# Kernel optimization log

Measured on AMD Instinct MI355X. Metric: run time of the kernel, lower is better.

The kernel has to match this reference:

```python
import jax, jax.numpy as jnp
import numpy as np

NUM_HEADS = 32
NUM_KV = 8
Q_MULT = NUM_HEADS // NUM_KV  # 4
HEAD_DIM = 128
WINDOW = 1024
SM_SCALE = 1.0 / np.sqrt(HEAD_DIM)


def setup_inputs() -> dict:
    key = jax.random.key(0)
    k1, k2, k3, k4 = jax.random.split(key, 4)
    B, S = 2, 2048
    Q = jax.random.normal(k1, (B, S, NUM_HEADS * HEAD_DIM), dtype=jnp.float32)
    K = jax.random.normal(k2, (B, S, NUM_KV * HEAD_DIM), dtype=jnp.float32)
    V = jax.random.normal(k3, (B, S, NUM_KV * HEAD_DIM), dtype=jnp.float32)
    sinks = jax.random.normal(k4, (NUM_HEADS,), dtype=jnp.float32) * 0.1
    return {"Q": Q, "K": K, "V": V, "sinks": sinks}


def reference(Q, K, V, sinks):
    B, S, _ = Q.shape
    # GQA layout: head = kv * q_mult + m (matches Q[b].view(S, kv, q_mult, d))
    Qh = Q.reshape(B, S, NUM_KV, Q_MULT, HEAD_DIM)
    Kh = K.reshape(B, S, NUM_KV, HEAD_DIM)
    Vh = V.reshape(B, S, NUM_KV, HEAD_DIM)

    # scores: [B, kv, q_mult, S_q, S_k]
    scores = jnp.einsum('bqhmd,bkhd->bhmqk', Qh, Kh) * SM_SCALE

    q_idx = jnp.arange(S)[:, None]
    k_idx = jnp.arange(S)[None, :]
    # causal AND within sliding window: q - WINDOW < k <= q
    allowed = (k_idx <= q_idx) & (k_idx > q_idx - WINDOW)
    scores = jnp.where(allowed[None, None, None, :, :], scores, -jnp.inf)

    # learned sink logit per head, appended as an extra softmax column
    sink = sinks.reshape(NUM_KV, Q_MULT)[None, :, :, None, None]
    sink = jnp.broadcast_to(sink, (B, NUM_KV, Q_MULT, S, 1))
    logits = jnp.concatenate([scores, sink], axis=-1)
    w = jax.nn.softmax(logits, axis=-1)[..., :-1]  # drop sink column

    out = jnp.einsum('bhmqk,bkhd->bqhmd', w, Vh)
    return out.reshape(B, S, NUM_HEADS * HEAD_DIM)
```

## Files before the change

### kernel.cpp

```cpp
#include <hip/hip_runtime.h>
#include <stdint.h>

#define S_LEN 2048
#define HD    128
#define NKV   8
#define NQM   4
#define WIN   1024
#define QB    32
#define KTILE 32
#define KVROW (NKV * HD)
#define QROW  (NQM * NKV * HD)

typedef __attribute__((ext_vector_type(8))) short bf16x8;
typedef __attribute__((ext_vector_type(4))) float f32x4;
typedef __attribute__((ext_vector_type(4))) int   i32x4;

__device__ __forceinline__ uint32_t cvtpk(float lo, float hi) {
  uint32_t r;
  asm("v_cvt_pk_bf16_f32 %0, %1, %2" : "=v"(r) : "v"(lo), "v"(hi));
  return r;
}
__device__ __forceinline__ uint32_t perm2(uint32_t a, uint32_t b, uint32_t sel) {
  uint32_t r;
  asm("v_perm_b32 %0, %1, %2, %3" : "=v"(r) : "v"(a), "v"(b), "s"(sel));
  return r;
}

__device__ __forceinline__ void load8bf(const uint16_t* p, uint32_t o[4]) {
  i32x4 v = *reinterpret_cast<const i32x4*>(p);
  o[0] = (uint32_t)v[0]; o[1] = (uint32_t)v[1]; o[2] = (uint32_t)v[2]; o[3] = (uint32_t)v[3];
}
__device__ __forceinline__ void load8bf(const float* p, uint32_t o[4]) {
  float4 a = *reinterpret_cast<const float4*>(p);
  float4 b = *reinterpret_cast<const float4*>(p + 4);
  o[0] = cvtpk(a.x, a.y);
  o[1] = cvtpk(a.z, a.w);
  o[2] = cvtpk(b.x, b.y);
  o[3] = cvtpk(b.z, b.w);
}

__global__ void cvt2_kernel(const float* __restrict__ inK, const float* __restrict__ inV,
                            uint16_t* __restrict__ outK, uint16_t* __restrict__ outV, int n4) {
  int i = blockIdx.x * blockDim.x + threadIdx.x;
  int stride = gridDim.x * blockDim.x;
  for (int j = i; j < 2 * n4; j += stride) {
    const float* in = (j < n4) ? inK : inV;
    uint16_t* out   = (j < n4) ? outK : outV;
    int jj = (j < n4) ? j : j - n4;
    float4 v = reinterpret_cast<const float4*>(in)[jj];
    uint2 o;
    o.x = cvtpk(v.x, v.y);
    o.y = cvtpk(v.z, v.w);
    reinterpret_cast<uint2*>(out)[jj] = o;
  }
}

#define VSWZ(d) (((((uint32_t)(d) >> 3) ^ (uint32_t)(d)) & 7u) << 3)

#define KPERM(a)  ((((a) >> 2) & 3) * 8 + ((a) >> 4) * 4 + ((a) & 3))
#define KPERMI(k) ((((k) >> 2) & 1) * 16 + ((k) >> 3) * 4 + ((k) & 3))

template <typename KVT>
__launch_bounds__(256, 2)
__global__ void attn_kernel(const float* __restrict__ Q,
                            const KVT* __restrict__ Ksrc,
                            const KVT* __restrict__ Vsrc,
                            const float* __restrict__ sinks,
                            float* __restrict__ out) {
  __shared__ __align__(16) uint8_t smem[32768];

  const int tid  = threadIdx.x;
  const int lane = tid & 63;
  const int wv   = tid >> 6;
  const int c    = lane & 15;
  const int g    = lane >> 4;

  const int bid = blockIdx.x;
  const int kv  = bid & 7;
  const int i2  = bid >> 3;
  const int b   = i2 / 48;
  const int pairIdx = i2 % 48;
  const int head = kv * NQM + wv;
  const float sink_l2 = sinks[head] * 1.4426950408889634f;

  int qtA, qtB, nrep;
  if (pairIdx < 16) { qtA = 31 - pairIdx; qtB = pairIdx; nrep = 2; }
  else              { qtA = pairIdx + 16; qtB = 0;       nrep = 1; }

  const size_t kbase = (size_t)(b * S_LEN) * KVROW + kv * HD;
  uint32_t kgo[2];
  #pragma unroll
  for (int ch = 0; ch < 2; ++ch) {
    const int o    = wv * 2048 + ch * 1024 + lane * 16;
    const int row  = o >> 8;
    const int key  = KPERM(row);
    const int scol = (o & 255) ^ ((row & 7) << 4);
    kgo[ch] = (uint32_t)(key * (KVROW * 2) + scol);
  }
  const int kr  = tid >> 3;
  const int kcB = (tid & 7) * 32;
  const int kpr = KPERMI(kr);
  const uint32_t kw0 = (uint32_t)(kpr * 256 + ((kcB)      ^ ((kpr & 7) << 4)));
  const uint32_t kw1 = (uint32_t)(kpr * 256 + ((kcB + 16) ^ ((kpr & 7) << 4)));
  const KVT* kg = Ksrc + kbase + (tid & 7) * 16;
  const int va = tid >> 4;
  const int vd = tid & 15;
  const KVT* vg = Vsrc + kbase + vd * 8;

  uint32_t vr0[4], vr1[4];

  auto stageK = [&](uint8_t* kbuf, int kt) {
    if constexpr (sizeof(KVT) == 2) {
      const uint8_t* kb = (const uint8_t*)(Ksrc + kbase) + (size_t)kt * (KVROW * 2);
      #pragma unroll
      for (int ch = 0; ch < 2; ++ch) {
        __builtin_amdgcn_global_load_lds(
            (const __attribute__((address_space(1))) void*)(kb + kgo[ch]),
            (__attribute__((address_space(3))) void*)(kbuf + wv * 2048 + ch * 1024),
            16, 0, 0);
      }
    } else {
      const KVT* src = kg + (size_t)(kt + kr) * KVROW;
      uint32_t t0[4], t1[4];
      load8bf(src, t0); load8bf(src + 8, t1);
      i32x4 w0, w1;
      w0[0]=(int)t0[0]; w0[1]=(int)t0[1]; w0[2]=(int)t0[2]; w0[3]=(int)t0[3];
      w1[0]=(int)t1[0]; w1[1]=(int)t1[1]; w1[2]=(int)t1[2]; w1[3]=(int)t1[3];
      *reinterpret_cast<i32x4*>(kbuf + kw0) = w0;
      *reinterpret_cast<i32x4*>(kbuf + kw1) = w1;
    }
  };
  auto loadV = [&](int kt) {
    const KVT* vs = vg + (size_t)(kt + 2 * va) * KVROW;
    load8bf(vs, vr0); load8bf(vs + KVROW, vr1);
  };
  auto writeV = [&](uint8_t* vbuf) {
    #pragma unroll
    for (int ii = 0; ii < 8; ++ii) {
      int d = vd * 8 + ii;
      uint32_t w = (ii & 1) ? perm2(vr1[ii >> 1], vr0[ii >> 1], 0x07060302u)
                            : perm2(vr1[ii >> 1], vr0[ii >> 1], 0x05040100u);
      uint32_t byte = (uint32_t)(d * 64) + (((uint32_t)(va * 4)) ^ VSWZ(d));
      *reinterpret_cast<uint32_t*>(vbuf + byte) = w;
    }
  };

  const float SCALE2 = 0.08838834764831845f * 1.4426950408889634f;

  for (int rep = 0; rep < nrep; ++rep) {
    const int q0 = (rep ? qtB : qtA) * QB;

    bf16x8 qf[2][4];
    #pragma unroll
    for (int tq = 0; tq < 2; ++tq) {
      const float* qp = Q + (size_t)(b * S_LEN + q0 + tq * 16 + c) * QROW + head * HD;
      #pragma unroll
      for (int f = 0; f < 4; ++f) {
        int d0 = f * 32 + g * 8;
        float4 a = *reinterpret_cast<const float4*>(qp + d0);
        float4 bb = *reinterpret_cast<const float4*>(qp + d0 + 4);
        i32x4 t;
        t[0] = (int)cvtpk(a.x * SCALE2, a.y * SCALE2);
        t[1] = (int)cvtpk(a.z * SCALE2, a.w * SCALE2);
        t[2] = (int)cvtpk(bb.x * SCALE2, bb.y * SCALE2);
        t[3] = (int)cvtpk(bb.z * SCALE2, bb.w * SCALE2);
        qf[tq][f] = __builtin_bit_cast(bf16x8, t);
      }
    }

    float m_[2] = {sink_l2, sink_l2};
    float lp_[2] = {0.25f, 0.25f};
    f32x4 acc[2][8];
    #pragma unroll
    for (int tq = 0; tq < 2; ++tq)
      #pragma unroll
      for (int dt = 0; dt < 8; ++dt) acc[tq][dt] = (f32x4)0.0f;

    int kstart = q0 - (WIN - 1);
    if (kstart < 0) kstart = 0;
    kstart &= ~(KTILE - 1);

    uint8_t* kcur = smem;         uint8_t* kalt = smem + 8192;
    uint8_t* vcur = smem + 16384; uint8_t* valt = smem + 24576;

    loadV(kstart);
    stageK(kcur, kstart);
    writeV(vcur);
    __syncthreads();

    for (int kt = kstart; kt <= q0; kt += KTILE) {
      const int ktn = (kt + KTILE <= q0) ? (kt + KTILE) : kt;
      stageK(kalt, ktn);
      loadV(ktn);

      f32x4 st[2][2];
      #pragma unroll
      for (int a_ = 0; a_ < 2; ++a_)
        #pragma unroll
        for (int b_ = 0; b_ < 2; ++b_) st[a_][b_] = (f32x4)0.0f;

      __builtin_amdgcn_s_setprio(1);
      #pragma unroll
      for (int kt_ = 0; kt_ < 2; ++kt_) {
        bf16x8 kf[4];
        #pragma unroll
        for (int f = 0; f < 4; ++f) {
          int row = kt_ * 16 + c;
          uint32_t byte = (uint32_t)(row * 256 + ((f * 64 + g * 16) ^ ((row & 7) << 4)));
          kf[f] = *reinterpret_cast<const bf16x8*>(kcur + byte);
        }
        #pragma unroll
        for (int tq = 0; tq < 2; ++tq)
          #pragma unroll
          for (int f = 0; f < 4; ++f)
            st[kt_][tq] = __builtin_amdgcn_mfma_f32_16x16x32_bf16(kf[f], qf[tq][f], st[kt_][tq], 0, 0, 0);
      }
      __builtin_amdgcn_s_setprio(0);

      const bool need_mask = (kt + KTILE - 1 > q0) || (kt < q0 + QB - WIN);
      if (need_mask) {
        #pragma unroll
        for (int kt_ = 0; kt_ < 2; ++kt_)
          #pragma unroll
          for (int tq = 0; tq < 2; ++tq)
            #pragma unroll
            for (int r = 0; r < 4; ++r) {
              int k_ = kt + g * 8 + kt_ * 4 + r;
              int q_ = q0 + tq * 16 + c;
              bool ok = (k_ <= q_) && (k_ > q_ - WIN);
              if (!ok) st[kt_][tq][r] = -1e38f;
            }
      }

      bf16x8 pa[2];
      #pragma unroll
      for (int tq = 0; tq < 2; ++tq) {
        float ownmax = fmaxf(fmaxf(fmaxf(st[0][tq][0], st[0][tq][1]), fmaxf(st[0][tq][2], st[0][tq][3])),
                             fmaxf(fmaxf(st[1][tq][0], st[1][tq][1]), fmaxf(st[1][tq][2], st[1][tq][3])));
        const float mold = m_[tq];
        if (!__all(ownmax <= mold + 11.54f)) {
          float vmax = fmaxf(ownmax, __shfl_xor(ownmax, 16));
          vmax = fmaxf(vmax, __shfl_xor(vmax, 32));
          float mnew = fmaxf(mold, vmax);
          float scl  = exp2f(mold - mnew);
          m_[tq] = mnew;
          lp_[tq] *= scl;
          float sc[4];
          #pragma unroll
          for (int r = 0; r < 4; ++r) sc[r] = __shfl(scl, (lane & 48) | (g * 4 + r));
          #pragma unroll
          for (int dt = 0; dt < 8; ++dt)
            #pragma unroll
            for (int r = 0; r < 4; ++r) acc[tq][dt][r] *= sc[r];
        }
        const float mrun = m_[tq];
        float p[2][4];
        float s = 0.0f;
        #pragma unroll
        for (int kt_ = 0; kt_ < 2; ++kt_)
          #pragma unroll
          for (int r = 0; r < 4; ++r) {
            float e = exp2f(st[kt_][tq][r] - mrun);
            p[kt_][r] = e;
            s += e;
          }
        lp_[tq] += s;
        i32x4 pv;
        pv[0] = (int)cvtpk(p[0][0], p[0][1]);
        pv[1] = (int)cvtpk(p[0][2], p[0][3]);
        pv[2] = (int)cvtpk(p[1][0], p[1][1]);
        pv[3] = (int)cvtpk(p[1][2], p[1][3]);
        pa[tq] = __builtin_bit_cast(bf16x8, pv);
      }

      __builtin_amdgcn_s_setprio(1);
      #pragma unroll
      for (int dt = 0; dt < 8; ++dt) {
        int d = dt * 16 + c;
        uint32_t rowb = (uint32_t)(d * 64);
        uint32_t swz  = VSWZ(d);
        uint2 lo = *reinterpret_cast<const uint2*>(vcur + rowb + (((uint32_t)(g * 16))     ^ swz));
        uint2 hi = *reinterpret_cast<const uint2*>(vcur + rowb + (((uint32_t)(g * 16 + 8)) ^ swz));
        i32x4 vv; vv[0] = (int)lo.x; vv[1] = (int)lo.y; vv[2] = (int)hi.x; vv[3] = (int)hi.y;
        bf16x8 vf = __builtin_bit_cast(bf16x8, vv);
        #pragma unroll
        for (int tq = 0; tq < 2; ++tq)
          acc[tq][dt] = __builtin_amdgcn_mfma_f32_16x16x32_bf16(pa[tq], vf, acc[tq][dt], 0, 0, 0);
      }
      __builtin_amdgcn_s_setprio(0);

      writeV(valt);
      __syncthreads();
      uint8_t* t0 = kcur; kcur = kalt; kalt = t0;
      uint8_t* t1 = vcur; vcur = valt; valt = t1;
    }

    #pragma unroll
    for (int tq = 0; tq < 2; ++tq) {
      float lt = lp_[tq];
      lt += __shfl_xor(lt, 16);
      lt += __shfl_xor(lt, 32);
      float linv = 1.0f / lt;
      float li[4];
      #pragma unroll
      for (int r = 0; r < 4; ++r) li[r] = __shfl(linv, (lane & 48) | (g * 4 + r));
      #pragma unroll
      for (int dt = 0; dt < 8; ++dt)
        #pragma unroll
        for (int r = 0; r < 4; ++r) {
          size_t o = (size_t)(b * S_LEN + q0 + tq * 16 + g * 4 + r) * QROW + head * HD + dt * 16 + c;
          out[o] = acc[tq][dt][r] * li[r];
        }
    }
  }
}

extern "C" void kernel_launch(void* const* d_in, const int* in_sizes, int n_in,
                              void* d_out, int out_size, void* d_ws, size_t ws_size,
                              hipStream_t stream) {
  const float* Q     = (const float*)d_in[0];
  const float* K     = (const float*)d_in[1];
  const float* V     = (const float*)d_in[2];
  const float* sinks = (const float*)d_in[3];
  float* out = (float*)d_out;

  const int nK = in_sizes[1];
  const int B  = in_sizes[0] / (S_LEN * QROW);
  dim3 grid(384 * B);

  const size_t need = (size_t)nK * 2u * 2u;
  if (ws_size >= need) {
    uint16_t* Kb = (uint16_t*)d_ws;
    uint16_t* Vb = Kb + nK;
    cvt2_kernel<<<1024, 256, 0, stream>>>(K, V, Kb, Vb, nK / 4);
    attn_kernel<uint16_t><<<grid, 256, 0, stream>>>(Q, Kb, Vb, sinks, out);
  } else {
    attn_kernel<float><<<grid, 256, 0, stream>>>(Q, K, V, sinks, out);
  }
}
```

Measured before the change: 219.1 us.

## Stage V via direct global-to-LDS loads and read with transposing LDS loads

V tiles are now copied straight from global memory into LDS with global_load_lds, in a new row layout, replacing the register round trip that used byte permutes and scattered 32-bit stores. The PV MFMA operands are then read with ds_read_b64_tr_b16 transposing LDS loads, software-pipelined one step ahead with explicit lgkmcnt waits. The aim is to cut VALU and LDS-write work and register pressure in the main loop. The hand-written waitcnt and sched barriers add scheduling rigidity, and the bf16 path relies on the new layout matching the transpose read pattern exactly.

```diff
diff --git a/kernel.cpp b/kernel.cpp
--- a/kernel.cpp
+++ b/kernel.cpp
@@ -14,15 +14,11 @@
 typedef __attribute__((ext_vector_type(8))) short bf16x8;
 typedef __attribute__((ext_vector_type(4))) float f32x4;
 typedef __attribute__((ext_vector_type(4))) int   i32x4;
+typedef __attribute__((ext_vector_type(2))) unsigned u32x2;
 
 __device__ __forceinline__ uint32_t cvtpk(float lo, float hi) {
   uint32_t r;
   asm("v_cvt_pk_bf16_f32 %0, %1, %2" : "=v"(r) : "v"(lo), "v"(hi));
-  return r;
-}
-__device__ __forceinline__ uint32_t perm2(uint32_t a, uint32_t b, uint32_t sel) {
-  uint32_t r;
-  asm("v_perm_b32 %0, %1, %2, %3" : "=v"(r) : "v"(a), "v"(b), "s"(sel));
   return r;
 }
 
@@ -55,10 +51,9 @@
   }
 }
 
-#define VSWZ(d) (((((uint32_t)(d) >> 3) ^ (uint32_t)(d)) & 7u) << 3)
-
 #define KPERM(a)  ((((a) >> 2) & 3) * 8 + ((a) >> 4) * 4 + ((a) & 3))
 #define KPERMI(k) ((((k) >> 2) & 1) * 16 + ((k) >> 3) * 4 + ((k) & 3))
+
 
 template <typename KVT>
 __launch_bounds__(256, 2)
@@ -97,6 +92,18 @@
     const int scol = (o & 255) ^ ((row & 7) << 4);
     kgo[ch] = (uint32_t)(key * (KVROW * 2) + scol);
   }
+  uint32_t vgo[2];
+  #pragma unroll
+  for (int ch = 0; ch < 2; ++ch) {
+    const int o16 = wv * 128 + ch * 64 + lane;
+    const int c0  = (o16 & 1) * 8;
+    const int j   = (o16 >> 1) & 3;
+    const int g_  = (o16 >> 3) & 3;
+    const int h   = (o16 >> 5) & 1;
+    const int D   = o16 >> 6;
+    const int k   = g_ * 8 + h * 4 + j;
+    vgo[ch] = (uint32_t)((k * KVROW + D * 16 + c0) * 2);
+  }
   const int kr  = tid >> 3;
   const int kcB = (tid & 7) * 32;
   const int kpr = KPERMI(kr);
@@ -107,7 +114,8 @@
   const int vd = tid & 15;
   const KVT* vg = Vsrc + kbase + vd * 8;
 
-  uint32_t vr0[4], vr1[4];
+  const uint32_t vlane =
+      (uint32_t)(uintptr_t)(__attribute__((address_space(3))) uint8_t*)(smem + 16384) + lane * 8;
 
   auto stageK = [&](uint8_t* kbuf, int kt) {
     if constexpr (sizeof(KVT) == 2) {
@@ -130,18 +138,30 @@
       *reinterpret_cast<i32x4*>(kbuf + kw1) = w1;
     }
   };
-  auto loadV = [&](int kt) {
-    const KVT* vs = vg + (size_t)(kt + 2 * va) * KVROW;
-    load8bf(vs, vr0); load8bf(vs + KVROW, vr1);
-  };
-  auto writeV = [&](uint8_t* vbuf) {
-    #pragma unroll
-    for (int ii = 0; ii < 8; ++ii) {
-      int d = vd * 8 + ii;
-      uint32_t w = (ii & 1) ? perm2(vr1[ii >> 1], vr0[ii >> 1], 0x07060302u)
-                            : perm2(vr1[ii >> 1], vr0[ii >> 1], 0x05040100u);
-      uint32_t byte = (uint32_t)(d * 64) + (((uint32_t)(va * 4)) ^ VSWZ(d));
-      *reinterpret_cast<uint32_t*>(vbuf + byte) = w;
+  auto stageV = [&](uint8_t* vbuf, int kt) {
+    if constexpr (sizeof(KVT) == 2) {
+      const uint8_t* vb = (const uint8_t*)(Vsrc + kbase) + (size_t)kt * (KVROW * 2);
+      #pragma unroll
+      for (int ch = 0; ch < 2; ++ch) {
+        __builtin_amdgcn_global_load_lds(
+            (const __attribute__((address_space(1))) void*)(vb + vgo[ch]),
+            (__attribute__((address_space(3))) void*)(vbuf + wv * 2048 + ch * 1024),
+            16, 0, 0);
+      }
+    } else {
+      const KVT* vs = vg + (size_t)(kt + 2 * va) * KVROW;
+      uint32_t r0[4], r1[4];
+      load8bf(vs, r0); load8bf(vs + KVROW, r1);
+      const int D = vd >> 1, half = (vd & 1) * 16;
+      const int k0 = 2 * va, k1 = k0 + 1;
+      auto offB = [&](int k) {
+        return (uint32_t)((D * 512 + ((k >> 2) & 1) * 256 + (k >> 3) * 64 + (k & 3) * 16) * 2 + half);
+      };
+      i32x4 w0, w1;
+      w0[0]=(int)r0[0]; w0[1]=(int)r0[1]; w0[2]=(int)r0[2]; w0[3]=(int)r0[3];
+      w1[0]=(int)r1[0]; w1[1]=(int)r1[1]; w1[2]=(int)r1[2]; w1[3]=(int)r1[3];
+      *reinterpret_cast<i32x4*>(vbuf + offB(k0)) = w0;
+      *reinterpret_cast<i32x4*>(vbuf + offB(k1)) = w1;
     }
   };
 
@@ -182,16 +202,16 @@
 
     uint8_t* kcur = smem;         uint8_t* kalt = smem + 8192;
     uint8_t* vcur = smem + 16384; uint8_t* valt = smem + 24576;
-
-    loadV(kstart);
+    uint32_t voff = 0;
+
     stageK(kcur, kstart);
-    writeV(vcur);
+    stageV(vcur, kstart);
     __syncthreads();
 
     for (int kt = kstart; kt <= q0; kt += KTILE) {
       const int ktn = (kt + KTILE <= q0) ? (kt + KTILE) : kt;
       stageK(kalt, ktn);
-      loadV(ktn);
+      stageV(valt, ktn);
 
       f32x4 st[2][2];
       #pragma unroll
@@ -273,26 +293,58 @@
         pa[tq] = __builtin_bit_cast(bf16x8, pv);
       }
 
-      __builtin_amdgcn_s_setprio(1);
-      #pragma unroll
-      for (int dt = 0; dt < 8; ++dt) {
-        int d = dt * 16 + c;
-        uint32_t rowb = (uint32_t)(d * 64);
-        uint32_t swz  = VSWZ(d);
-        uint2 lo = *reinterpret_cast<const uint2*>(vcur + rowb + (((uint32_t)(g * 16))     ^ swz));
-        uint2 hi = *reinterpret_cast<const uint2*>(vcur + rowb + (((uint32_t)(g * 16 + 8)) ^ swz));
-        i32x4 vv; vv[0] = (int)lo.x; vv[1] = (int)lo.y; vv[2] = (int)hi.x; vv[3] = (int)hi.y;
-        bf16x8 vf = __builtin_bit_cast(bf16x8, vv);
-        #pragma unroll
-        for (int tq = 0; tq < 2; ++tq)
-          acc[tq][dt] = __builtin_amdgcn_mfma_f32_16x16x32_bf16(pa[tq], vf, acc[tq][dt], 0, 0, 0);
-      }
-      __builtin_amdgcn_s_setprio(0);
-
-      writeV(valt);
+      if constexpr (sizeof(KVT) == 2) {
+        const uint32_t vaddr = vlane + voff;
+        __builtin_amdgcn_s_setprio(1);
+        __builtin_amdgcn_sched_barrier(0);
+        #define TR16(OFF) ({ u32x2 _r;                                                   \
+            asm volatile("ds_read_b64_tr_b16 %0, %1 offset:%c2"                          \
+                         : "=v"(_r) : "v"(vaddr), "i"(OFF)); _r; })
+        u32x2 h0 = TR16(0), h1 = TR16(512);
+        u32x2 n0, n1;
+        #define PV_STEP(dt, LAST)                                                        \
+          {                                                                              \
+            if (!(LAST)) { n0 = TR16(((dt) + 1) * 1024); n1 = TR16(((dt) + 1) * 1024 + 512); } \
+            asm volatile("s_waitcnt lgkmcnt(%c0)" :: "i"((LAST) ? 0 : 2) : "memory");    \
+            __builtin_amdgcn_sched_barrier(0);                                           \
+            i32x4 vv; vv[0]=(int)h0.x; vv[1]=(int)h0.y; vv[2]=(int)h1.x; vv[3]=(int)h1.y; \
+            bf16x8 vf = __builtin_bit_cast(bf16x8, vv);                                  \
+            acc[0][dt] = __builtin_amdgcn_mfma_f32_16x16x32_bf16(pa[0], vf, acc[0][dt], 0, 0, 0); \
+            acc[1][dt] = __builtin_amdgcn_mfma_f32_16x16x32_bf16(pa[1], vf, acc[1][dt], 0, 0, 0); \
+            h0 = n0; h1 = n1;                                                            \
+          }
+        PV_STEP(0,0) PV_STEP(1,0) PV_STEP(2,0) PV_STEP(3,0)
+        PV_STEP(4,0) PV_STEP(5,0) PV_STEP(6,0) PV_STEP(7,1)
+        #undef PV_STEP
+        #undef TR16
+        __builtin_amdgcn_s_setprio(0);
+      } else {
+        __builtin_amdgcn_s_setprio(1);
+        #pragma unroll
+        for (int dt = 0; dt < 8; ++dt) {
+          uint16_t e[8];
+          #pragma unroll
+          for (int jj = 0; jj < 8; ++jj) {
+            uint32_t off = (uint32_t)((dt * 512 + (jj >> 2) * 256 + g * 64 + (jj & 3) * 16 + c) * 2);
+            e[jj] = *reinterpret_cast<const uint16_t*>(vcur + off);
+          }
+          i32x4 vv;
+          vv[0] = (int)((uint32_t)e[0] | ((uint32_t)e[1] << 16));
+          vv[1] = (int)((uint32_t)e[2] | ((uint32_t)e[3] << 16));
+          vv[2] = (int)((uint32_t)e[4] | ((uint32_t)e[5] << 16));
+          vv[3] = (int)((uint32_t)e[6] | ((uint32_t)e[7] << 16));
+          bf16x8 vf = __builtin_bit_cast(bf16x8, vv);
+          #pragma unroll
+          for (int tq = 0; tq < 2; ++tq)
+            acc[tq][dt] = __builtin_amdgcn_mfma_f32_16x16x32_bf16(pa[tq], vf, acc[tq][dt], 0, 0, 0);
+        }
+        __builtin_amdgcn_s_setprio(0);
+      }
+
       __syncthreads();
       uint8_t* t0 = kcur; kcur = kalt; kalt = t0;
       uint8_t* t1 = vcur; vcur = valt; valt = t1;
+      voff ^= 8192;
     }
 
     #pragma unroll
```

Result: faster. 200.1 us (-8.7%).
